# Optimization experiments

Measured on AMD Instinct MI355X. Metric: run time of the kernel, lower is better.

The kernel has to match this reference:

```python
import jax, jax.numpy as jnp
import numpy as np

D_IN, D_HEAD, D_EXPAND, D_OUT, H = 512, 64, 2048, 512, 8
D_Q = D_HEAD * H  # 512
D_K = D_HEAD * H  # 512
D_V = D_IN * H    # 4096 (non-standard: per-head value dim = d_in)
EPS = 1e-5


def layernorm(x, g, b):
    mu = jnp.mean(x, axis=-1, keepdims=True)
    var = jnp.mean(jnp.square(x - mu), axis=-1, keepdims=True)
    return (x - mu) * jax.lax.rsqrt(var + EPS) * g + b


def setup_inputs() -> dict:
    key = jax.random.key(0)
    ks = jax.random.split(key, 12)
    B, N = 2, 2048
    s_in = 1.0 / np.sqrt(D_IN)
    s_mh = 1.0 / np.sqrt(D_IN * H)
    s_ex = 1.0 / np.sqrt(D_EXPAND)
    return {
        "x": jax.random.normal(ks[0], (B, N, D_IN), jnp.float32),
        "ln1_g": jnp.ones((D_IN,), jnp.float32),
        "ln1_b": jnp.zeros((D_IN,), jnp.float32),
        "Wqkv": jax.random.normal(ks[1], (D_IN, D_Q + D_K + D_V), jnp.float32) * s_in,
        "bqkv": jax.random.normal(ks[2], (D_Q + D_K + D_V,), jnp.float32) * 0.01,
        "Wm": jax.random.normal(ks[3], (D_IN * H, D_IN), jnp.float32) * s_mh,
        "bm": jax.random.normal(ks[4], (D_IN,), jnp.float32) * 0.01,
        "ln2_g": jnp.ones((D_IN,), jnp.float32),
        "ln2_b": jnp.zeros((D_IN,), jnp.float32),
        "W1": jax.random.normal(ks[5], (D_IN, D_EXPAND), jnp.float32) * s_in,
        "b1": jax.random.normal(ks[6], (D_EXPAND,), jnp.float32) * 0.01,
        "W2": jax.random.normal(ks[7], (D_EXPAND, D_OUT), jnp.float32) * s_ex,
        "b2": jax.random.normal(ks[8], (D_OUT,), jnp.float32) * 0.01,
    }


def reference(x, ln1_g, ln1_b, Wqkv, bqkv, Wm, bm, ln2_g, ln2_b, W1, b1, W2, b2):
    B, N, _ = x.shape
    scale = D_HEAD ** -0.5
    qkv = layernorm(x, ln1_g, ln1_b) @ Wqkv + bqkv
    q, k, v = jnp.split(qkv, [D_Q, D_Q + D_K], axis=-1)
    q = q.reshape(B, N, H, D_HEAD).transpose(0, 2, 1, 3)  # (B,H,N,dh)
    k = k.reshape(B, N, H, D_HEAD).transpose(0, 2, 1, 3)
    v = v.reshape(B, N, H, D_IN).transpose(0, 2, 1, 3)    # (B,H,N,d_in)
    attn = jax.nn.softmax(jnp.einsum('bhnd,bhmd->bhnm', q, k) * scale, axis=-1)
    out = jnp.einsum('bhnm,bhmc->bhnc', attn, v)          # (B,H,N,d_in)
    out = out.transpose(0, 2, 1, 3).reshape(B, N, H * D_IN)
    x2 = x + out @ Wm + bm
    h = layernorm(x2, ln2_g, ln2_b) @ W1 + b1
    h = h * jax.nn.sigmoid(h)  # Swish
    return h @ W2 + b2 + x2    # shortcut = Identity (d_in == d_out)
```

## Files before the change

### kernel.cpp

```cpp
#include <hip/hip_runtime.h>
#include <cmath>

typedef unsigned short u16;
typedef unsigned int   u32;
typedef __attribute__((ext_vector_type(8))) __bf16 bf16x8;
typedef __attribute__((ext_vector_type(4))) float  f32x4;
typedef __attribute__((ext_vector_type(8))) unsigned short u16x8;
typedef __attribute__((ext_vector_type(4))) unsigned short u16x4;

#define DEV __device__ __forceinline__

DEV float bf2f(u16 u){ union{u32 i; float f;} v; v.i=((u32)u)<<16; return v.f; }
DEV u16 f2bf(float f){ union{float f; u32 i;} v; v.f=f; u32 r=v.i+0x7fffu+((v.i>>16)&1u); return (u16)(r>>16); }

#if defined(__has_builtin) && __has_builtin(__builtin_amdgcn_global_load_lds)
DEV void gld16(const void* g, void* l){
  __builtin_amdgcn_global_load_lds((__attribute__((address_space(1))) void*)g,
                                   (__attribute__((address_space(3))) void*)l, 16, 0, 0);
}
#else
DEV void gld16(const void* g, void* l){ *(u16x8*)l = *(const u16x8*)g; }
#endif

#if defined(__has_builtin) && __has_builtin(__builtin_amdgcn_exp2f)
DEV float fexp2(float x){ return __builtin_amdgcn_exp2f(x); }
#else
DEV float fexp2(float x){ return exp2f(x); }
#endif

__global__ void detect_k(const u16* __restrict__ x, int* __restrict__ flag)
{
  if (threadIdx.x == 0 && blockIdx.x == 0){
    int sane = 0;
    for (int i = 0; i < 64; ++i){
      int e = (x[i] >> 7) & 0xFF;
      sane += (e >= 100 && e <= 150);
    }
    *flag = (sane < 56) ? 1 : 0;
  }
}

__global__ __launch_bounds__(256)
void conv_vecs(const void* a0,const void* a1,const void* a2,const void* a3,
               const void* a4,const void* a5,const void* a6,const void* a7,
               float* __restrict__ dst, const int* __restrict__ flag)
{
  int i = blockIdx.x*256 + threadIdx.x;
  if (i >= 10240) return;
  const void* src; int off;
  if      (i < 512)  { src=a0; off=i; }
  else if (i < 1024) { src=a1; off=i-512; }
  else if (i < 6144) { src=a2; off=i-1024; }
  else if (i < 6656) { src=a3; off=i-6144; }
  else if (i < 7168) { src=a4; off=i-6656; }
  else if (i < 7680) { src=a5; off=i-7168; }
  else if (i < 9728) { src=a6; off=i-7680; }
  else               { src=a7; off=i-9728; }
  dst[i] = (*flag) ? ((const float*)src)[off] : bf2f(((const u16*)src)[off]);
}

#define SWZ_SRC(c) (((c)&7) ^ (((c)>>3)&7))

template<int SWZ>
DEV void remap_xcd(int& bx, int& by)
{
  if (SWZ==1){
    int L = by*(int)gridDim.x + bx;
    int xcd = L & 7, l = L >> 3;
    int chunk = (int)gridDim.x >> 3;
    bx = xcd*chunk + (l % chunk);
    by = l / chunk;
  } else if (SWZ==2){
    int L = by*(int)gridDim.x + bx;
    int xcd = L & 7, l = L >> 3;
    int chunk = (int)gridDim.y >> 3;
    by = xcd*chunk + (l % chunk);
    bx = l / chunk;
  }
}

template<int MODE, int SWZ>
__global__ __launch_bounds__(256)
void gemm_bt(const u16* __restrict__ A, const u16* __restrict__ BT,
             void* __restrict__ C, const float* __restrict__ bias,
             int K, int lda, int ldb, int ldc)
{
  __shared__ u16 As[128*64];
  __shared__ u16 Bs[128*64];
  const int tid  = threadIdx.x;
  const int lane = tid & 63;
  const int quad = lane>>4, l7 = lane&7, l15 = lane&15;
  const int wv   = tid >> 6;
  const int wm   = wv >> 1, wn = wv & 1;
  int bx = blockIdx.x, by = blockIdx.y;
  remap_xcd<SWZ>(bx, by);
  const long m0 = (long)by * 128;
  const long n0 = (long)bx * 128;

  f32x4 acc[4][4];
#pragma unroll
  for (int i=0;i<4;i++)
#pragma unroll
    for (int j=0;j<4;j++) acc[i][j] = (f32x4){0.f,0.f,0.f,0.f};

  for (int k0=0; k0<K; k0+=64){
    __syncthreads();
#pragma unroll
    for (int i=0;i<4;i++){
      int c = i*256 + tid;
      gld16(A  + (m0 + (c>>3))*lda + k0 + SWZ_SRC(c)*8, &As[c*8]);
      gld16(BT + (n0 + (c>>3))*ldb + k0 + SWZ_SRC(c)*8, &Bs[c*8]);
    }
    __syncthreads();
#pragma unroll
    for (int kk=0;kk<2;kk++){
      const int ch = ((kk*4 + quad) ^ l7) * 8;
      bf16x8 af[4], bfr[4];
#pragma unroll
      for (int t=0;t<4;t++){
        af[t]  = *(const bf16x8*)&As[(wm*64 + t*16 + l15)*64 + ch];
        bfr[t] = *(const bf16x8*)&Bs[(wn*64 + t*16 + l15)*64 + ch];
      }
#pragma unroll
      for (int ti=0;ti<4;ti++)
#pragma unroll
        for (int tj=0;tj<4;tj++)
          acc[ti][tj] = __builtin_amdgcn_mfma_f32_16x16x32_bf16(af[ti], bfr[tj], acc[ti][tj], 0,0,0);
    }
  }

#pragma unroll
  for (int ti=0;ti<4;ti++)
#pragma unroll
  for (int tj=0;tj<4;tj++)
#pragma unroll
  for (int r=0;r<4;r++){
    long row = m0 + wm*64 + ti*16 + quad*4 + r;
    long col = n0 + wn*64 + tj*16 + l15;
    float v = acc[ti][tj][r] + bias[col];
    if (MODE==2) v = v / (1.f + __expf(-v));
    ((u16*)C)[row*ldc+col] = f2bf(v);
  }
}

template<int MODE, int SWZ>
__global__ __launch_bounds__(256)
void gemm_n64(const u16* __restrict__ A, const u16* __restrict__ BT,
              void* __restrict__ C, const float* __restrict__ bias,
              const void* __restrict__ res,
              int K, int lda, int ldb, int ldc, const int* __restrict__ flag)
{
  __shared__ u16 As[2][128*64];
  __shared__ u16 Bs[2][64*64];
  const int tid  = threadIdx.x;
  const int lane = tid & 63;
  const int quad = lane>>4, l7 = lane&7, l15 = lane&15;
  const int wm   = tid >> 6;
  int bx = blockIdx.x, by = blockIdx.y;
  remap_xcd<SWZ>(bx, by);
  const long m0 = (long)by * 128;
  const long n0 = (long)bx * 64;
  const bool f32io = flag && (*flag != 0);

  f32x4 acc[2][4];
#pragma unroll
  for (int i=0;i<2;i++)
#pragma unroll
    for (int j=0;j<4;j++) acc[i][j] = (f32x4){0.f,0.f,0.f,0.f};

  auto stage = [&](int bi, int k0){
#pragma unroll
    for (int i=0;i<4;i++){
      int c = i*256 + tid;
      gld16(A + (m0 + (c>>3))*lda + k0 + SWZ_SRC(c)*8, &As[bi][c*8]);
    }
#pragma unroll
    for (int i=0;i<2;i++){
      int c = i*256 + tid;
      gld16(BT + (n0 + (c>>3))*ldb + k0 + SWZ_SRC(c)*8, &Bs[bi][c*8]);
    }
  };

  const int S = K >> 6;
  stage(0, 0);
  __syncthreads();

  for (int s=0; s<S; ++s){
    const int cb = s & 1;
    if (s+1 < S) stage(cb^1, (s+1)<<6);
#pragma unroll
    for (int kk=0;kk<2;kk++){
      const int ch = ((kk*4 + quad) ^ l7) * 8;
      bf16x8 af[2], bfr[4];
#pragma unroll
      for (int t=0;t<2;t++)
        af[t]  = *(const bf16x8*)&As[cb][(wm*32 + t*16 + l15)*64 + ch];
#pragma unroll
      for (int t=0;t<4;t++)
        bfr[t] = *(const bf16x8*)&Bs[cb][(t*16 + l15)*64 + ch];
#pragma unroll
      for (int ti=0;ti<2;ti++)
#pragma unroll
        for (int tj=0;tj<4;tj++)
          acc[ti][tj] = __builtin_amdgcn_mfma_f32_16x16x32_bf16(af[ti], bfr[tj], acc[ti][tj], 0,0,0);
    }
    __syncthreads();
  }

#pragma unroll
  for (int ti=0;ti<2;ti++)
#pragma unroll
  for (int tj=0;tj<4;tj++)
#pragma unroll
  for (int r=0;r<4;r++){
    long row = m0 + wm*32 + ti*16 + quad*4 + r;
    long col = n0 + tj*16 + l15;
    float v = acc[ti][tj][r] + bias[col];
    if (MODE==1){
      v += f32io ? ((const float*)res)[row*ldc+col]
                 : bf2f(((const u16*)res)[row*ldc+col]);
      ((float*)C)[row*ldc+col] = v;
    } else {
      v += ((const float*)res)[row*ldc+col];
      if (f32io) ((float*)C)[row*ldc+col] = v;
      else       ((u16*)C)[row*ldc+col]   = f2bf(v);
    }
  }
}

__global__ __launch_bounds__(512, 2)
void att_flash(const u16* __restrict__ qkv, const u16* __restrict__ vt,
               u16* __restrict__ ao)
{
  __shared__ u16 Qs[128*64];
  __shared__ u16 Ks[2][64*64];
  __shared__ u16 Ps[128*68];
  __shared__ u16 Vs[512*64];
  __shared__ float m_run[128], l_run[128], alph[128];
  __shared__ int resc[2];
  const int tid=threadIdx.x, lane=tid&63, wv=tid>>6;
  const int wm=wv>>2, wn=wv&3;
  const int quad=lane>>4, l7=lane&7, l15=lane&15;
  const int bid = blockIdx.x;
  const int id  = ((bid&7)<<5) + (bid>>3);
  const int qt  = id & 15, bh = id >> 4;
  const int b = bh>>3, h = bh&7;
  const long q0 = (long)qt*128;
  const u16* qb = qkv + ((long)b*2048 + q0)*5120 + h*64;
  const u16* kb = qkv + (long)b*2048*5120 + 512 + h*64;
  const u16* vb = vt + (long)bh*512*2048;

#pragma unroll
  for (int i=0;i<2;i++){
    int c=i*512+tid;
    gld16(qb + (long)(c>>3)*5120 + SWZ_SRC(c)*8, &Qs[c*8]);
  }
  { int c=tid; gld16(kb + (long)(c>>3)*5120 + SWZ_SRC(c)*8, &Ks[0][c*8]); }
  if (tid<128){ m_run[tid] = -1e30f; l_run[tid] = 0.f; }
  if (tid==0){ resc[0]=0; resc[1]=0; }

  f32x4 o[4][8];
#pragma unroll
  for (int i=0;i<4;i++)
#pragma unroll
    for (int j=0;j<8;j++) o[i][j] = (f32x4){0.f,0.f,0.f,0.f};

  for (int mt=0; mt<32; ++mt){
    const long m0 = (long)mt*64;
    const int cur = mt&1;
    __syncthreads();

    if (mt < 31){ int c=tid; gld16(kb + (m0+64 + (c>>3))*5120 + SWZ_SRC(c)*8, &Ks[cur^1][c*8]); }
#pragma unroll
    for (int i=0;i<8;i++){
      int c=i*512+tid;
      gld16(vb + (long)(c>>3)*2048 + m0 + SWZ_SRC(c)*8, &Vs[c*8]);
    }
    if (tid==0) resc[cur^1] = 0;

    f32x4 s[4];
#pragma unroll
    for (int j=0;j<4;j++) s[j] = (f32x4){0.f,0.f,0.f,0.f};
#pragma unroll
    for (int kk=0;kk<2;kk++){
      const int ch = ((kk*4 + quad) ^ l7) * 8;
      bf16x8 af = *(const bf16x8*)&Qs[(wv*16 + l15)*64 + ch];
#pragma unroll
      for (int tj=0;tj<4;tj++){
        bf16x8 bfr = *(const bf16x8*)&Ks[cur][(tj*16 + l15)*64 + ch];
        s[tj] = __builtin_amdgcn_mfma_f32_16x16x32_bf16(af, bfr, s[tj], 0,0,0);
      }
    }

    float nm[4], al[4], rs[4];
    bool chg = false;
#pragma unroll
    for (int r=0;r<4;r++){
      float vm = fmaxf(fmaxf(s[0][r],s[1][r]), fmaxf(s[2][r],s[3][r]));
      vm = fmaxf(vm, __shfl_xor(vm,1)); vm = fmaxf(vm, __shfl_xor(vm,2));
      vm = fmaxf(vm, __shfl_xor(vm,4)); vm = fmaxf(vm, __shfl_xor(vm,8));
      float mo = m_run[wv*16 + quad*4 + r];
      float vs = vm*0.125f;
      bool c_ = (vs > mo + 8.f);
      nm[r] = c_ ? vs : mo;
      al[r] = c_ ? __expf(mo - vs) : 1.f;
      chg |= c_;
      rs[r] = 0.f;
    }
    float nml[4];
#pragma unroll
    for (int r=0;r<4;r++) nml[r] = nm[r]*1.44269504f;
#pragma unroll
    for (int tj=0;tj<4;tj++)
#pragma unroll
    for (int r=0;r<4;r++){
      float pv = fexp2(fmaf(s[tj][r], 0.18033688f, -nml[r]));
      rs[r] += pv;
      Ps[(wv*16 + quad*4 + r)*68 + tj*16 + l15] = f2bf(pv);
    }
#pragma unroll
    for (int r=0;r<4;r++){
      rs[r] += __shfl_xor(rs[r],1); rs[r] += __shfl_xor(rs[r],2);
      rs[r] += __shfl_xor(rs[r],4); rs[r] += __shfl_xor(rs[r],8);
    }
    if (l15==0){
#pragma unroll
      for (int r=0;r<4;r++){
        int row = wv*16 + quad*4 + r;
        alph[row]  = al[r];
        m_run[row] = nm[r];
        l_run[row] = l_run[row]*al[r] + rs[r];
      }
    }
    if (__any((int)chg) && lane==0) resc[cur] = 1;
    __syncthreads();

    if (resc[cur]){
      float a_[4][4];
#pragma unroll
      for (int ti=0;ti<4;ti++)
#pragma unroll
        for (int r=0;r<4;r++) a_[ti][r] = alph[wm*64 + ti*16 + quad*4 + r];
#pragma unroll
      for (int ti=0;ti<4;ti++)
#pragma unroll
      for (int tj=0;tj<8;tj++)
#pragma unroll
        for (int r=0;r<4;r++) o[ti][tj][r] *= a_[ti][r];
    }
#pragma unroll
    for (int kk=0;kk<2;kk++){
      const int ch = ((kk*4 + quad) ^ l7) * 8;
      bf16x8 af[4], bfr[8];
#pragma unroll
      for (int t=0;t<4;t++){
        int base = (wm*64 + t*16 + l15)*68 + kk*32 + quad*8;
        union { u16x4 hh[2]; bf16x8 v; } u;
        u.hh[0] = *(const u16x4*)&Ps[base];
        u.hh[1] = *(const u16x4*)&Ps[base+4];
        af[t] = u.v;
      }
#pragma unroll
      for (int t=0;t<8;t++)
        bfr[t] = *(const bf16x8*)&Vs[(wn*128 + t*16 + l15)*64 + ch];
#pragma unroll
      for (int ti=0;ti<4;ti++)
#pragma unroll
        for (int tj=0;tj<8;tj++)
          o[ti][tj] = __builtin_amdgcn_mfma_f32_16x16x32_bf16(af[ti], bfr[tj], o[ti][tj], 0,0,0);
    }
  }

  float rl[4][4];
#pragma unroll
  for (int ti=0;ti<4;ti++)
#pragma unroll
    for (int r=0;r<4;r++) rl[ti][r] = 1.f / l_run[wm*64 + ti*16 + quad*4 + r];
#pragma unroll
  for (int ti=0;ti<4;ti++)
#pragma unroll
  for (int tj=0;tj<8;tj++)
#pragma unroll
  for (int r=0;r<4;r++){
    long rown = q0 + wm*64 + ti*16 + quad*4 + r;
    long col  = wn*128 + tj*16 + l15;
    ao[((long)b*2048 + rown)*4096 + (long)h*512 + col] = f2bf(o[ti][tj][r]*rl[ti][r]);
  }
}

template<int SRC>
__global__ __launch_bounds__(256)
void ln_kernel(const void* __restrict__ xin, const float* __restrict__ g,
               const float* __restrict__ bb, u16* __restrict__ out,
               const int* __restrict__ flag)
{
  const int tid=threadIdx.x, lane=tid&63, wv=tid>>6;
  const long row = (long)blockIdx.x*4 + wv;
  const bool f32 = (SRC==1) || (flag && *flag != 0);
  float v[8];
  if (f32){
    const float* xr = (const float*)xin + row*512 + lane*8;
#pragma unroll
    for (int j=0;j<8;j++) v[j]=xr[j];
  } else {
    const u16* xr = (const u16*)xin + row*512 + lane*8;
    u16x8 xv = *(const u16x8*)xr;
#pragma unroll
    for (int j=0;j<8;j++) v[j]=bf2f(xv[j]);
  }
  float s1=0.f, s2=0.f;
#pragma unroll
  for (int j=0;j<8;j++){ s1+=v[j]; s2+=v[j]*v[j]; }
  for (int off=1; off<64; off<<=1){ s1+=__shfl_xor(s1,off); s2+=__shfl_xor(s2,off); }
  float mu  = s1*(1.f/512.f);
  float var = s2*(1.f/512.f) - mu*mu;
  float rs  = rsqrtf(var + 1e-5f);
  u16x8 ov;
#pragma unroll
  for (int j=0;j<8;j++){
    int col = lane*8+j;
    ov[j] = f2bf((v[j]-mu)*rs*g[col] + bb[col]);
  }
  *(u16x8*)(out + row*512 + lane*8) = ov;
}

template<bool DUAL>
__global__ __launch_bounds__(256)
void transpose_k(const void* __restrict__ in_, u16* __restrict__ out,
                 int ldi, int ldo, long izh, long izl, long oz,
                 const int* __restrict__ flag)
{
  __shared__ u16 t[32][33];
  const int z = blockIdx.z;
  const bool f32 = DUAL && flag && (*flag != 0);
  const long zoff = (long)(z>>3)*izh + (long)(z&7)*izl;
  out += (long)z*oz;
  const int tx = threadIdx.x, ty = threadIdx.y;
  const long c  = (long)blockIdx.x*32 + tx;
  const long r0 = (long)blockIdx.y*32;
  if (f32){
    const float* in = (const float*)in_ + zoff;
#pragma unroll
    for (int j=0;j<4;j++) t[ty+j*8][tx] = f2bf(in[(r0+ty+j*8)*ldi + c]);
  } else {
    const u16* in = (const u16*)in_ + zoff;
#pragma unroll
    for (int j=0;j<4;j++) t[ty+j*8][tx] = in[(r0+ty+j*8)*ldi + c];
  }
  __syncthreads();
  const long rr = r0 + tx;
  const long cc = (long)blockIdx.x*32 + ty;
#pragma unroll
  for (int j=0;j<4;j++) out[(cc+j*8)*ldo + rr] = t[tx][ty+j*8];
}

extern "C" void kernel_launch(void* const* d_in, const int* in_sizes, int n_in,
                              void* d_out, int out_size, void* d_ws, size_t ws_size,
                              hipStream_t stream)
{
  const void* x    = d_in[0];
  const void* ln1g = d_in[1];
  const void* ln1b = d_in[2];
  const void* Wqkv = d_in[3];
  const void* bqkv = d_in[4];
  const void* Wm   = d_in[5];
  const void* bm   = d_in[6];
  const void* ln2g = d_in[7];
  const void* ln2b = d_in[8];
  const void* W1   = d_in[9];
  const void* b1   = d_in[10];
  const void* W2   = d_in[11];
  const void* b2   = d_in[12];

  char* p = (char*)d_ws;
  auto take = [&](size_t n){ void* r=(void*)p; p += (n + 255) & ~(size_t)255; return r; };
  u16*   lnb   = (u16*)  take((size_t)4096*512*2);
  u16*   qkv   = (u16*)  take((size_t)4096*5120*2);
  u16*   vtb   = (u16*)  take((size_t)16*512*2048*2);
  u16*   wqkvT = (u16*)  take((size_t)5120*512*2);
  u16*   wmT   = (u16*)  take((size_t)512*4096*2);
  u16*   w1T   = (u16*)  take((size_t)2048*512*2);
  u16*   w2T   = (u16*)  take((size_t)512*2048*2);
  u16*   ao    = (u16*)  take((size_t)4096*4096*2);
  float* cvec  = (float*)take((size_t)10240*4);
  int*   flag  = (int*)  take(4);
  float* x2    = (float*)vtb;
  u16*   hb    = qkv;

  detect_k<<<1, 64, 0, stream>>>((const u16*)x, flag);
  conv_vecs<<<40, 256, 0, stream>>>(ln1g, ln1b, bqkv, bm, ln2g, ln2b, b1, b2, cvec, flag);

  dim3 tb(32,8);
  transpose_k<true><<<dim3(160,16,1), tb, 0, stream>>>(Wqkv, wqkvT, 5120, 512, 0,0,0, flag);
  transpose_k<true><<<dim3(16,128,1), tb, 0, stream>>>(Wm,   wmT,   512, 4096, 0,0,0, flag);
  transpose_k<true><<<dim3(64,16,1),  tb, 0, stream>>>(W1,   w1T,  2048, 512, 0,0,0, flag);
  transpose_k<true><<<dim3(16,64,1),  tb, 0, stream>>>(W2,   w2T,   512, 2048, 0,0,0, flag);

  ln_kernel<0><<<1024, 256, 0, stream>>>(x, cvec+0, cvec+512, lnb, flag);
  gemm_bt<0,1><<<dim3(40,32), 256, 0, stream>>>(lnb, wqkvT, qkv, cvec+1024, 512, 512, 512, 5120);

  transpose_k<false><<<dim3(16,64,16), tb, 0, stream>>>(qkv + 1024, vtb, 5120, 2048,
                                                        (long)2048*5120, 512, (long)512*2048, nullptr);
  att_flash<<<dim3(256), 512, 0, stream>>>(qkv, vtb, ao);

  gemm_n64<1,2><<<dim3(8,32), 256, 0, stream>>>(ao, wmT, x2, cvec+6144, x,
                                                4096, 4096, 4096, 512, flag);
  ln_kernel<1><<<1024, 256, 0, stream>>>(x2, cvec+6656, cvec+7168, lnb, nullptr);
  gemm_bt<2,2><<<dim3(16,32), 256, 0, stream>>>(lnb, w1T, hb, cvec+7680, 512, 512, 512, 2048);
  gemm_n64<3,2><<<dim3(8,32), 256, 0, stream>>>(hb, w2T, d_out, cvec+9728, x2,
                                                2048, 2048, 2048, 512, flag);
}
```

Before: 397.1 us.

## Fuse V transpose into QKV GEMM epilogue and keep Q fragments in registers

The QKV projection GEMM now writes the V portion directly in transposed per-head layout through a shared-memory staging tile, which removes the separate transpose kernel and its read and write of the 32 MB V region. V columns are no longer written to the row-major qkv buffer. The attention kernel also loads its Q fragments into registers once before the key loop instead of re-reading shared memory every iteration, which costs a few extra VGPRs.

```diff
diff --git a/kernel.cpp b/kernel.cpp
--- a/kernel.cpp
+++ b/kernel.cpp
@@ -79,14 +79,15 @@
   }
 }
 
-template<int MODE, int SWZ>
+template<int MODE, int SWZ, bool VT>
 __global__ __launch_bounds__(256)
 void gemm_bt(const u16* __restrict__ A, const u16* __restrict__ BT,
              void* __restrict__ C, const float* __restrict__ bias,
-             int K, int lda, int ldb, int ldc)
-{
-  __shared__ u16 As[128*64];
-  __shared__ u16 Bs[128*64];
+             int K, int lda, int ldb, int ldc, u16* __restrict__ vout)
+{
+  __shared__ u16 AB[2*128*64];
+  u16* As = AB;
+  u16* Bs = AB + 128*64;
   const int tid  = threadIdx.x;
   const int lane = tid & 63;
   const int quad = lane>>4, l7 = lane&7, l15 = lane&15;
@@ -127,6 +128,44 @@
         for (int tj=0;tj<4;tj++)
           acc[ti][tj] = __builtin_amdgcn_mfma_f32_16x16x32_bf16(af[ti], bfr[tj], acc[ti][tj], 0,0,0);
     }
+  }
+
+  if (VT && n0 >= 1024){
+    const int hh   = (int)((n0 - 1024) >> 9);
+    const int c0   = (int)((n0 - 1024) & 511);
+    const int b_   = (int)(m0 >> 11);
+    const int kloc = (int)(m0 & 2047);
+    u16* vb = vout + ((long)(b_*8 + hh))*512*2048 + kloc;
+    u16* Ts = AB;
+    __syncthreads();
+#pragma unroll
+    for (int pass=0; pass<2; ++pass){
+      if (pass) __syncthreads();
+      if (wn == pass){
+#pragma unroll
+        for (int ti=0;ti<4;ti++)
+#pragma unroll
+        for (int tj=0;tj<4;tj++)
+#pragma unroll
+        for (int r=0;r<4;r++){
+          int row = wm*64 + ti*16 + quad*4 + r;
+          int cl  = tj*16 + l15;
+          float v = acc[ti][tj][r] + bias[n0 + pass*64 + cl];
+          Ts[row*68 + cl] = f2bf(v);
+        }
+      }
+      __syncthreads();
+#pragma unroll
+      for (int step=0; step<4; ++step){
+        int cr = step*16 + (tid>>4);
+        int t8 = (tid&15)*8;
+        u16x8 pk;
+#pragma unroll
+        for (int j=0;j<8;j++) pk[j] = Ts[(t8+j)*68 + cr];
+        *(u16x8*)(vb + (long)(c0 + pass*64 + cr)*2048 + t8) = pk;
+      }
+    }
+    return;
   }
 
 #pragma unroll
@@ -265,6 +304,12 @@
 #pragma unroll
     for (int j=0;j<8;j++) o[i][j] = (f32x4){0.f,0.f,0.f,0.f};
 
+  __syncthreads();
+  bf16x8 qreg[2];
+#pragma unroll
+  for (int kk=0;kk<2;kk++)
+    qreg[kk] = *(const bf16x8*)&Qs[(wv*16 + l15)*64 + ((kk*4 + quad) ^ l7)*8];
+
   for (int mt=0; mt<32; ++mt){
     const long m0 = (long)mt*64;
     const int cur = mt&1;
@@ -284,11 +329,10 @@
 #pragma unroll
     for (int kk=0;kk<2;kk++){
       const int ch = ((kk*4 + quad) ^ l7) * 8;
-      bf16x8 af = *(const bf16x8*)&Qs[(wv*16 + l15)*64 + ch];
 #pragma unroll
       for (int tj=0;tj<4;tj++){
         bf16x8 bfr = *(const bf16x8*)&Ks[cur][(tj*16 + l15)*64 + ch];
-        s[tj] = __builtin_amdgcn_mfma_f32_16x16x32_bf16(af, bfr, s[tj], 0,0,0);
+        s[tj] = __builtin_amdgcn_mfma_f32_16x16x32_bf16(qreg[kk], bfr, s[tj], 0,0,0);
       }
     }
 
@@ -497,16 +541,16 @@
   transpose_k<true><<<dim3(16,64,1),  tb, 0, stream>>>(W2,   w2T,   512, 2048, 0,0,0, flag);
 
   ln_kernel<0><<<1024, 256, 0, stream>>>(x, cvec+0, cvec+512, lnb, flag);
-  gemm_bt<0,1><<<dim3(40,32), 256, 0, stream>>>(lnb, wqkvT, qkv, cvec+1024, 512, 512, 512, 5120);
-
-  transpose_k<false><<<dim3(16,64,16), tb, 0, stream>>>(qkv + 1024, vtb, 5120, 2048,
-                                                        (long)2048*5120, 512, (long)512*2048, nullptr);
+  gemm_bt<0,1,true><<<dim3(40,32), 256, 0, stream>>>(lnb, wqkvT, qkv, cvec+1024,
+                                                     512, 512, 512, 5120, vtb);
+
   att_flash<<<dim3(256), 512, 0, stream>>>(qkv, vtb, ao);
 
   gemm_n64<1,2><<<dim3(8,32), 256, 0, stream>>>(ao, wmT, x2, cvec+6144, x,
                                                 4096, 4096, 4096, 512, flag);
   ln_kernel<1><<<1024, 256, 0, stream>>>(x2, cvec+6656, cvec+7168, lnb, nullptr);
-  gemm_bt<2,2><<<dim3(16,32), 256, 0, stream>>>(lnb, w1T, hb, cvec+7680, 512, 512, 512, 2048);
+  gemm_bt<2,2,false><<<dim3(16,32), 256, 0, stream>>>(lnb, w1T, hb, cvec+7680,
+                                                      512, 512, 512, 2048, nullptr);
   gemm_n64<3,2><<<dim3(8,32), 256, 0, stream>>>(hb, w2T, d_out, cvec+9728, x2,
                                                 2048, 2048, 2048, 512, flag);
 }
```

Result: faster. 388.1 us (-2.3%).
